# Performance work log

Measured on AMD Instinct MI355X. Metric: run time of the kernel, lower is better.

## Reference

```python
import jax, jax.numpy as jnp
import numpy as np

W_DIM = 512
LRELU_SLOPE = 0.2
ACT_GAIN = np.sqrt(2.0).astype(np.float32)  # def_gain for lrelu, gain=1


def setup_inputs() -> dict:
    key = jax.random.key(0)
    k1, k2, k3, k4 = jax.random.split(key, 4)
    B, Cin, Cout, R, K = 8, 128, 128, 32, 3
    return {
        "x": jax.random.normal(k1, (B, Cin, R, R, R), dtype=jnp.float32),
        "w": jax.random.normal(k2, (B, W_DIM), dtype=jnp.float32),
        "weight": jax.random.normal(k3, (Cout, Cin, K, K, K), dtype=jnp.float32),
        "affine_weight": jax.random.normal(k4, (Cin, W_DIM), dtype=jnp.float32),
        "affine_bias": jnp.ones((Cin,), dtype=jnp.float32),
        "bias": jnp.zeros((Cout,), dtype=jnp.float32),
    }


def _conv_one(xi, wi):
    # xi: [Cin, D, H, W], wi: [Cout, Cin, k, k, k] -> [Cout, D, H, W]
    return jax.lax.conv_general_dilated(
        xi[None], wi, window_strides=(1, 1, 1),
        padding=[(1, 1), (1, 1), (1, 1)],
        dimension_numbers=("NCDHW", "OIDHW", "NCDHW"))[0]


def reference(x, w, weight, affine_weight, affine_bias, bias):
    B = x.shape[0]
    # affine: FullyConnectedLayer, linear, weight_gain = 1/sqrt(w_dim), bias_gain=1
    styles = w @ (affine_weight * (1.0 / np.sqrt(W_DIM))).T + affine_bias  # [B, Cin]
    # modulate
    wmod = weight[None] * styles[:, None, :, None, None, None]  # [B, Cout, Cin, k, k, k]
    # demodulate
    dcoefs = jax.lax.rsqrt(jnp.sum(jnp.square(wmod), axis=(2, 3, 4, 5)) + 1e-8)  # [B, Cout]
    wmod = wmod * dcoefs[:, :, None, None, None, None]
    # grouped conv (groups = batch) == vmap of per-sample conv
    out = jax.vmap(_conv_one)(x, wmod)  # [B, Cout, R, R, R]
    # bias_act: lrelu with gain=sqrt(2), clamp=None (noise path is disabled in forward)
    out = out + bias[None, :, None, None, None]
    out = jnp.where(out >= 0, out, out * LRELU_SLOPE) * ACT_GAIN
    return out
```

## Files before the change

kernel.cpp:

```cpp
#include <hip/hip_runtime.h>
#include <hip/hip_bf16.h>

typedef __attribute__((ext_vector_type(8))) short bf16x8;
typedef __attribute__((ext_vector_type(4))) float f32x4;

#define WDIM 512
#define CIN 128
#define COUT 128
#define NRES 32
#define NSP 32768
#define NTAPS 27

#define ROWB 2112
#define LDSROWS 16

#define ZP_OFF 4096
#define XT_OFF 8192
#define WM_OFF (8192 + 67108864)

typedef __attribute__((address_space(1))) const unsigned int gu32;
typedef __attribute__((address_space(3))) unsigned int lu32;

__global__ void k_styles(const float* __restrict__ w,
                         const float* __restrict__ aw,
                         const float* __restrict__ ab,
                         float* __restrict__ styles,
                         float* __restrict__ zeropad) {
  int b = blockIdx.x;
  int c = threadIdx.x;
  if (b == 0) {
#pragma unroll
    for (int i = 0; i < 8; i++) zeropad[i * 128 + c] = 0.f;
  }
  const float4* wr = (const float4*)(w + (size_t)b * WDIM);
  const float4* ar = (const float4*)(aw + (size_t)c * WDIM);
  float s = 0.f;
#pragma unroll 8
  for (int k = 0; k < WDIM / 4; k++) {
    float4 wv = wr[k], av = ar[k];
    s += wv.x * av.x + wv.y * av.y + wv.z * av.z + wv.w * av.w;
  }
  styles[b * CIN + c] = s * 0.04419417382415922f + ab[c];
}

__global__ void k_wmod(const float* __restrict__ weight,
                       const float* __restrict__ styles,
                       __hip_bfloat16* __restrict__ wmod) {
  int b = blockIdx.x >> 7;
  int co = blockIdx.x & 127;
  __shared__ float st[CIN];
  __shared__ float red[4];
  int tid = threadIdx.x;
  if (tid < CIN) st[tid] = styles[b * CIN + tid];
  __syncthreads();
  const float* wr = weight + (size_t)co * (CIN * NTAPS);
  float ss = 0.f;
  for (int o = tid; o < CIN * NTAPS; o += 256) {
    float v = wr[o] * st[o / NTAPS];
    ss += v * v;
  }
#pragma unroll
  for (int off = 32; off > 0; off >>= 1) ss += __shfl_down(ss, off);
  if ((tid & 63) == 0) red[tid >> 6] = ss;
  __syncthreads();
  float d = rsqrtf(red[0] + red[1] + red[2] + red[3] + 1e-8f);
  for (int o = tid; o < CIN * NTAPS; o += 256) {
    int t = o >> 7;
    int cin = o & 127;
    float v = wr[cin * NTAPS + t] * st[cin] * d;
    int cc = cin >> 5, cl = cin & 31;
    wmod[((((size_t)(b * 4 + cc) * COUT + co) * NTAPS + t) << 5) + cl] =
        __float2bfloat16(v);
  }
}

__global__ __launch_bounds__(256)
void k_xt(const float* __restrict__ x, __hip_bfloat16* __restrict__ xt) {
  __shared__ __align__(16) float ts[32][524];
  int t = threadIdx.x;
  int blk = blockIdx.x;
  int b = blk >> 8, cc = (blk >> 6) & 3, sp0 = (blk & 63) << 9;
  const float* xb = x + (size_t)b * CIN * NSP + (size_t)cc * 32 * NSP + sp0;
#pragma unroll
  for (int i = 0; i < 16; i++) {
    int idx = i * 256 + t;
    int cin = idx >> 7, spq = idx & 127;
    float4 v = *(const float4*)(xb + (size_t)cin * NSP + spq * 4);
    *(float4*)&ts[cin][spq * 4] = v;
  }
  __syncthreads();
  __hip_bfloat16* ob = xt + ((size_t)(b * 4 + cc) * NSP + sp0) * 32;
#pragma unroll
  for (int j = 0; j < 8; j++) {
    int chunk = j * 256 + t;
    int sp_l = chunk >> 2, q = chunk & 3;
    union { bf16x8 v; __hip_bfloat16 h[8]; } u;
#pragma unroll
    for (int k = 0; k < 8; k++) u.h[k] = __float2bfloat16(ts[q * 8 + k][sp_l]);
    *(bf16x8*)(ob + (size_t)sp_l * 32 + q * 8) = u.v;
  }
}

__global__ __launch_bounds__(128, 2)
void k_conv(const char* __restrict__ ws,
            const float* __restrict__ bias,
            float* __restrict__ out) {
  __shared__ __align__(16) char xs[LDSROWS * ROWB];

  int tid = threadIdx.x;
  int lane = tid & 63, w = tid >> 6;
  int l15 = lane & 15, g = lane >> 4;
  int blk = blockIdx.x;
  int b = blk & 7;
  int tile = blk >> 3;
  int z0 = (tile >> 4) * 2, y0 = (tile & 15) * 2;

  {
    int r16 = tid >> 3, c8 = (tid & 7) * 8;
    *(int2*)&xs[r16 * ROWB + 2048 + c8] = make_int2(0, 0);
  }

  int hxs = tid >> 2;
  int qs = (tid & 3) ^ ((hxs >> 1) & 3);
  int svoff = (hxs * 4 + qs) * 16;

  int vaddr[8][3];
#pragma unroll
  for (int ni = 0; ni < 8; ni++) {
    int row = (ni >> 2) * 4 + ((ni >> 1) & 1);
    int dx = (ni & 1) * 16 + l15;
#pragma unroll
    for (int tx = 0; tx < 3; tx++) {
      int hx = dx + tx - 1;
      int hxc = ((unsigned)hx > 31u) ? 32 : hx;
      int pos = g ^ ((hxc >> 1) & 3);
      vaddr[ni][tx] = row * ROWB + hxc * 64 + pos * 16;
    }
  }

  const bf16x8* ap = (const bf16x8*)(ws + WM_OFF);
  int abase[4];
#pragma unroll
  for (int mi = 0; mi < 4; mi++)
    abase[mi] = (w * 64 + mi * 16 + l15) * 108 + g;

  f32x4 acc[4][8];
#pragma unroll
  for (int mi = 0; mi < 4; mi++)
#pragma unroll
    for (int ni = 0; ni < 8; ni++) acc[mi][ni] = (f32x4){0.f, 0.f, 0.f, 0.f};

  const char* zpg = ws + ZP_OFF;
  const char* xtb = ws + XT_OFF + (size_t)b * (4 * NSP * 64);

#pragma unroll 1
  for (int cc = 0; cc < 4; cc++) {
    const char* xtc = xtb + (size_t)cc * (NSP * 64);
    int sab = ((b * 4 + cc) * 128) * 108;
    int abc0 = sab + abase[0], abc1 = sab + abase[1];
    int abc2 = sab + abase[2], abc3 = sab + abase[3];

    bf16x8 A[2][4], B0[4], B1[4];
    A[0][0] = ap[abc0]; A[0][1] = ap[abc1]; A[0][2] = ap[abc2]; A[0][3] = ap[abc3];
    __builtin_amdgcn_sched_barrier(0);

#pragma unroll
    for (int i = 0; i < 16; i++) {
      int zz = z0 + (i >> 2) - 1, yy = y0 + (i & 3) - 1;
      bool ok = ((unsigned)zz < NRES) & ((unsigned)yy < NRES);
      const char* base = ok ? (xtc + (long)((zz << 10) + (yy << 5)) * 64) : zpg;
      __builtin_amdgcn_global_load_lds((gu32*)(base + svoff),
                                       (lu32*)(xs + i * ROWB + w * 1024), 16, 0, 0);
    }
    __syncthreads();

#pragma unroll
    for (int j = 0; j < 4; j++) B0[j] = *(const bf16x8*)(xs + vaddr[j][0]);

#pragma unroll
    for (int t = 0; t < NTAPS; t++) {
      const int tz = t / 9, ty2 = (t / 3) % 3, txx = t % 3;
      const int lit = (tz * 4 + ty2) * ROWB;
      const int s = t & 1;
      if (t < NTAPS - 1) {
        const int t1 = t + 1;
        A[s ^ 1][0] = ap[abc0 + t1 * 4];
        A[s ^ 1][1] = ap[abc1 + t1 * 4];
        A[s ^ 1][2] = ap[abc2 + t1 * 4];
        A[s ^ 1][3] = ap[abc3 + t1 * 4];
      }
#pragma unroll
      for (int j = 0; j < 4; j++)
        B1[j] = *(const bf16x8*)(xs + vaddr[4 + j][txx] + lit);
      __builtin_amdgcn_s_setprio(1);
#pragma unroll
      for (int mi = 0; mi < 4; mi++) {
        acc[mi][0] = __builtin_amdgcn_mfma_f32_16x16x32_bf16(A[s][mi], B0[0], acc[mi][0], 0, 0, 0);
        acc[mi][1] = __builtin_amdgcn_mfma_f32_16x16x32_bf16(A[s][mi], B0[1], acc[mi][1], 0, 0, 0);
        acc[mi][2] = __builtin_amdgcn_mfma_f32_16x16x32_bf16(A[s][mi], B0[2], acc[mi][2], 0, 0, 0);
        acc[mi][3] = __builtin_amdgcn_mfma_f32_16x16x32_bf16(A[s][mi], B0[3], acc[mi][3], 0, 0, 0);
      }
      __builtin_amdgcn_s_setprio(0);
      if (t < NTAPS - 1) {
        const int t1 = t + 1;
        const int tz1 = t1 / 9, ty1 = (t1 / 3) % 3, tx1 = t1 % 3;
        const int lit1 = (tz1 * 4 + ty1) * ROWB;
#pragma unroll
        for (int j = 0; j < 4; j++)
          B0[j] = *(const bf16x8*)(xs + vaddr[j][tx1] + lit1);
      }
      __builtin_amdgcn_s_setprio(1);
#pragma unroll
      for (int mi = 0; mi < 4; mi++) {
        acc[mi][4] = __builtin_amdgcn_mfma_f32_16x16x32_bf16(A[s][mi], B1[0], acc[mi][4], 0, 0, 0);
        acc[mi][5] = __builtin_amdgcn_mfma_f32_16x16x32_bf16(A[s][mi], B1[1], acc[mi][5], 0, 0, 0);
        acc[mi][6] = __builtin_amdgcn_mfma_f32_16x16x32_bf16(A[s][mi], B1[2], acc[mi][6], 0, 0, 0);
        acc[mi][7] = __builtin_amdgcn_mfma_f32_16x16x32_bf16(A[s][mi], B1[3], acc[mi][7], 0, 0, 0);
      }
      __builtin_amdgcn_s_setprio(0);
    }
    if (cc < 3) __syncthreads();
  }

  size_t ob = ((size_t)(b * COUT + w * 64 + g * 4)) * NSP +
              (size_t)z0 * 1024 + (size_t)y0 * 32;
#pragma unroll
  for (int mi = 0; mi < 4; mi++) {
    float4 bsv = *(const float4*)(bias + w * 64 + mi * 16 + g * 4);
    float bs[4] = {bsv.x, bsv.y, bsv.z, bsv.w};
#pragma unroll
    for (int ni = 0; ni < 8; ni++) {
      int spo = (ni >> 2) * 1024 + ((ni >> 1) & 1) * 32 + (ni & 1) * 16 + l15;
#pragma unroll
      for (int r = 0; r < 4; r++) {
        float v = acc[mi][ni][r] + bs[r];
        v = (v >= 0.f ? v : v * 0.2f) * 1.41421356237309515f;
        out[ob + (size_t)(mi * 16 + r) * NSP + spo] = v;
      }
    }
  }
}

extern "C" void kernel_launch(void* const* d_in, const int* in_sizes, int n_in,
                              void* d_out, int out_size, void* d_ws, size_t ws_size,
                              hipStream_t stream) {
  const float* x      = (const float*)d_in[0];
  const float* w      = (const float*)d_in[1];
  const float* weight = (const float*)d_in[2];
  const float* aw     = (const float*)d_in[3];
  const float* ab     = (const float*)d_in[4];
  const float* bias   = (const float*)d_in[5];
  float* out = (float*)d_out;

  float* styles = (float*)d_ws;
  float* zeropad = (float*)((char*)d_ws + ZP_OFF);
  __hip_bfloat16* xt = (__hip_bfloat16*)((char*)d_ws + XT_OFF);
  __hip_bfloat16* wmod = (__hip_bfloat16*)((char*)d_ws + WM_OFF);

  k_styles<<<8, 128, 0, stream>>>(w, aw, ab, styles, zeropad);
  k_wmod<<<8 * 128, 256, 0, stream>>>(weight, styles, wmod);
  k_xt<<<8 * 4 * 64, 256, 0, stream>>>(x, xt);
  k_conv<<<8 * 256, 128, 0, stream>>>((const char*)d_ws, bias, out);
}
```

Measured before the change: 239.8 us.

## Switch conv inner loop from 16x16x32 to 32x32x16 bf16 MFMA tiles

New measurement: 273.7 us. 14.1% more time.

```diff
diff --git a/kernel.cpp b/kernel.cpp
--- a/kernel.cpp
+++ b/kernel.cpp
@@ -2,7 +2,7 @@
 #include <hip/hip_bf16.h>
 
 typedef __attribute__((ext_vector_type(8))) short bf16x8;
-typedef __attribute__((ext_vector_type(4))) float f32x4;
+typedef __attribute__((ext_vector_type(16))) float f32x16;
 
 #define WDIM 512
 #define CIN 128
@@ -109,7 +109,7 @@
 
   int tid = threadIdx.x;
   int lane = tid & 63, w = tid >> 6;
-  int l15 = lane & 15, g = lane >> 4;
+  int l31 = lane & 31, g2 = lane >> 5;
   int blk = blockIdx.x;
   int b = blk & 7;
   int tile = blk >> 3;
@@ -124,31 +124,32 @@
   int qs = (tid & 3) ^ ((hxs >> 1) & 3);
   int svoff = (hxs * 4 + qs) * 16;
 
-  int vaddr[8][3];
-#pragma unroll
-  for (int ni = 0; ni < 8; ni++) {
-    int row = (ni >> 2) * 4 + ((ni >> 1) & 1);
-    int dx = (ni & 1) * 16 + l15;
+  int vaddr[4][3];
+#pragma unroll
+  for (int ni = 0; ni < 4; ni++) {
+    int row = (ni >> 1) * 4 + (ni & 1);
 #pragma unroll
     for (int tx = 0; tx < 3; tx++) {
-      int hx = dx + tx - 1;
+      int hx = l31 + tx - 1;
       int hxc = ((unsigned)hx > 31u) ? 32 : hx;
-      int pos = g ^ ((hxc >> 1) & 3);
+      int pos = g2 ^ ((hxc >> 1) & 3);
       vaddr[ni][tx] = row * ROWB + hxc * 64 + pos * 16;
     }
   }
 
   const bf16x8* ap = (const bf16x8*)(ws + WM_OFF);
-  int abase[4];
-#pragma unroll
-  for (int mi = 0; mi < 4; mi++)
-    abase[mi] = (w * 64 + mi * 16 + l15) * 108 + g;
-
-  f32x4 acc[4][8];
-#pragma unroll
-  for (int mi = 0; mi < 4; mi++)
-#pragma unroll
-    for (int ni = 0; ni < 8; ni++) acc[mi][ni] = (f32x4){0.f, 0.f, 0.f, 0.f};
+  int abase[2];
+#pragma unroll
+  for (int mi = 0; mi < 2; mi++)
+    abase[mi] = (w * 64 + mi * 32 + l31) * 108 + g2;
+
+  f32x16 acc[2][4];
+#pragma unroll
+  for (int mi = 0; mi < 2; mi++)
+#pragma unroll
+    for (int ni = 0; ni < 4; ni++)
+#pragma unroll
+      for (int r = 0; r < 16; r++) acc[mi][ni][r] = 0.f;
 
   const char* zpg = ws + ZP_OFF;
   const char* xtb = ws + XT_OFF + (size_t)b * (4 * NSP * 64);
@@ -158,10 +159,10 @@
     const char* xtc = xtb + (size_t)cc * (NSP * 64);
     int sab = ((b * 4 + cc) * 128) * 108;
     int abc0 = sab + abase[0], abc1 = sab + abase[1];
-    int abc2 = sab + abase[2], abc3 = sab + abase[3];
-
-    bf16x8 A[2][4], B0[4], B1[4];
-    A[0][0] = ap[abc0]; A[0][1] = ap[abc1]; A[0][2] = ap[abc2]; A[0][3] = ap[abc3];
+
+    bf16x8 A[2][2][2], B[2][2][4];
+    A[0][0][0] = ap[abc0];     A[0][0][1] = ap[abc0 + 2];
+    A[0][1][0] = ap[abc1];     A[0][1][1] = ap[abc1 + 2];
     __builtin_amdgcn_sched_barrier(0);
 
 #pragma unroll
@@ -175,67 +176,74 @@
     __syncthreads();
 
 #pragma unroll
-    for (int j = 0; j < 4; j++) B0[j] = *(const bf16x8*)(xs + vaddr[j][0]);
+    for (int j = 0; j < 4; j++) {
+      B[0][0][j] = *(const bf16x8*)(xs + vaddr[j][0]);
+      B[0][1][j] = *(const bf16x8*)(xs + (vaddr[j][0] ^ 32));
+    }
 
 #pragma unroll
     for (int t = 0; t < NTAPS; t++) {
-      const int tz = t / 9, ty2 = (t / 3) % 3, txx = t % 3;
-      const int lit = (tz * 4 + ty2) * ROWB;
-      const int s = t & 1;
+      const int cur = t & 1, nxt = cur ^ 1;
+      const int t1 = t + 1;
+      const int tx1 = t1 % 3;
+      const int lit1 = ((t1 / 9) * 4 + (t1 / 3) % 3) * ROWB;
       if (t < NTAPS - 1) {
-        const int t1 = t + 1;
-        A[s ^ 1][0] = ap[abc0 + t1 * 4];
-        A[s ^ 1][1] = ap[abc1 + t1 * 4];
-        A[s ^ 1][2] = ap[abc2 + t1 * 4];
-        A[s ^ 1][3] = ap[abc3 + t1 * 4];
-      }
-#pragma unroll
-      for (int j = 0; j < 4; j++)
-        B1[j] = *(const bf16x8*)(xs + vaddr[4 + j][txx] + lit);
+        A[nxt][0][0] = ap[abc0 + t1 * 4];  A[nxt][0][1] = ap[abc0 + t1 * 4 + 2];
+        A[nxt][1][0] = ap[abc1 + t1 * 4];  A[nxt][1][1] = ap[abc1 + t1 * 4 + 2];
+      }
+      if (t < NTAPS - 1) {
+#pragma unroll
+        for (int j = 0; j < 4; j++)
+          B[nxt][0][j] = *(const bf16x8*)(xs + vaddr[j][tx1] + lit1);
+      }
       __builtin_amdgcn_s_setprio(1);
 #pragma unroll
-      for (int mi = 0; mi < 4; mi++) {
-        acc[mi][0] = __builtin_amdgcn_mfma_f32_16x16x32_bf16(A[s][mi], B0[0], acc[mi][0], 0, 0, 0);
-        acc[mi][1] = __builtin_amdgcn_mfma_f32_16x16x32_bf16(A[s][mi], B0[1], acc[mi][1], 0, 0, 0);
-        acc[mi][2] = __builtin_amdgcn_mfma_f32_16x16x32_bf16(A[s][mi], B0[2], acc[mi][2], 0, 0, 0);
-        acc[mi][3] = __builtin_amdgcn_mfma_f32_16x16x32_bf16(A[s][mi], B0[3], acc[mi][3], 0, 0, 0);
+      for (int mi = 0; mi < 2; mi++) {
+        acc[mi][0] = __builtin_amdgcn_mfma_f32_32x32x16_bf16(A[cur][mi][0], B[cur][0][0], acc[mi][0], 0, 0, 0);
+        acc[mi][1] = __builtin_amdgcn_mfma_f32_32x32x16_bf16(A[cur][mi][0], B[cur][0][1], acc[mi][1], 0, 0, 0);
+        acc[mi][2] = __builtin_amdgcn_mfma_f32_32x32x16_bf16(A[cur][mi][0], B[cur][0][2], acc[mi][2], 0, 0, 0);
+        acc[mi][3] = __builtin_amdgcn_mfma_f32_32x32x16_bf16(A[cur][mi][0], B[cur][0][3], acc[mi][3], 0, 0, 0);
       }
       __builtin_amdgcn_s_setprio(0);
       if (t < NTAPS - 1) {
-        const int t1 = t + 1;
-        const int tz1 = t1 / 9, ty1 = (t1 / 3) % 3, tx1 = t1 % 3;
-        const int lit1 = (tz1 * 4 + ty1) * ROWB;
 #pragma unroll
         for (int j = 0; j < 4; j++)
-          B0[j] = *(const bf16x8*)(xs + vaddr[j][tx1] + lit1);
+          B[nxt][1][j] = *(const bf16x8*)(xs + ((vaddr[j][tx1] + lit1) ^ 32));
       }
       __builtin_amdgcn_s_setprio(1);
 #pragma unroll
-      for (int mi = 0; mi < 4; mi++) {
-        acc[mi][4] = __builtin_amdgcn_mfma_f32_16x16x32_bf16(A[s][mi], B1[0], acc[mi][4], 0, 0, 0);
-        acc[mi][5] = __builtin_amdgcn_mfma_f32_16x16x32_bf16(A[s][mi], B1[1], acc[mi][5], 0, 0, 0);
-        acc[mi][6] = __builtin_amdgcn_mfma_f32_16x16x32_bf16(A[s][mi], B1[2], acc[mi][6], 0, 0, 0);
-        acc[mi][7] = __builtin_amdgcn_mfma_f32_16x16x32_bf16(A[s][mi], B1[3], acc[mi][7], 0, 0, 0);
+      for (int mi = 0; mi < 2; mi++) {
+        acc[mi][0] = __builtin_amdgcn_mfma_f32_32x32x16_bf16(A[cur][mi][1], B[cur][1][0], acc[mi][0], 0, 0, 0);
+        acc[mi][1] = __builtin_amdgcn_mfma_f32_32x32x16_bf16(A[cur][mi][1], B[cur][1][1], acc[mi][1], 0, 0, 0);
+        acc[mi][2] = __builtin_amdgcn_mfma_f32_32x32x16_bf16(A[cur][mi][1], B[cur][1][2], acc[mi][2], 0, 0, 0);
+        acc[mi][3] = __builtin_amdgcn_mfma_f32_32x32x16_bf16(A[cur][mi][1], B[cur][1][3], acc[mi][3], 0, 0, 0);
       }
       __builtin_amdgcn_s_setprio(0);
     }
     if (cc < 3) __syncthreads();
   }
 
-  size_t ob = ((size_t)(b * COUT + w * 64 + g * 4)) * NSP +
-              (size_t)z0 * 1024 + (size_t)y0 * 32;
-#pragma unroll
-  for (int mi = 0; mi < 4; mi++) {
-    float4 bsv = *(const float4*)(bias + w * 64 + mi * 16 + g * 4);
-    float bs[4] = {bsv.x, bsv.y, bsv.z, bsv.w};
-#pragma unroll
-    for (int ni = 0; ni < 8; ni++) {
-      int spo = (ni >> 2) * 1024 + ((ni >> 1) & 1) * 32 + (ni & 1) * 16 + l15;
-#pragma unroll
-      for (int r = 0; r < 4; r++) {
+  size_t ob0 = ((size_t)(b * COUT + w * 64 + 4 * g2)) * NSP +
+               (size_t)z0 * 1024 + (size_t)y0 * 32;
+#pragma unroll
+  for (int mi = 0; mi < 2; mi++) {
+    int cb = w * 64 + mi * 32 + 4 * g2;
+    float bs[16];
+#pragma unroll
+    for (int j = 0; j < 4; j++) {
+      float4 bv = *(const float4*)(bias + cb + j * 8);
+      bs[j * 4 + 0] = bv.x; bs[j * 4 + 1] = bv.y;
+      bs[j * 4 + 2] = bv.z; bs[j * 4 + 3] = bv.w;
+    }
+#pragma unroll
+    for (int ni = 0; ni < 4; ni++) {
+      int spo = (ni >> 1) * 1024 + (ni & 1) * 32 + l31;
+#pragma unroll
+      for (int r = 0; r < 16; r++) {
         float v = acc[mi][ni][r] + bs[r];
         v = (v >= 0.f ? v : v * 0.2f) * 1.41421356237309515f;
-        out[ob + (size_t)(mi * 16 + r) * NSP + spo] = v;
+        int co_off = mi * 32 + (r & 3) + 8 * (r >> 2);
+        out[ob0 + (size_t)co_off * NSP + spo] = v;
       }
     }
   }
```
